# Optimization experiments

Hardware: AMD Instinct MI355X
Metric: run time of the kernel (lower is better)

Reference implementation:

```python
import jax, jax.numpy as jnp
import numpy as np

N, E, IN_DIM, HID, HEADS, LAYERS, NTYPES, NGRAPH = 50000, 600000, 64, 128, 8, 3, 10, 500
C = HID // HEADS
NEG_SLOPE = 0.2
EPS = 1e-5


def setup_inputs() -> dict:
    key = jax.random.key(0)
    ks = jax.random.split(key, 24)
    inp = {
        "x": jax.random.normal(ks[0], (N, IN_DIM), jnp.float32),
        "edge_index": jax.random.randint(ks[1], (2, E), 0, N),
        "node_types": jax.random.randint(ks[2], (N,), 0, NTYPES),
        "batch": jnp.sort(jax.random.randint(ks[3], (N,), 0, NGRAPH)),
        # node embedding linear
        "emb_W": jax.random.normal(ks[4], (IN_DIM, HID), jnp.float32) / np.sqrt(IN_DIM),
        "emb_b": jnp.zeros((HID,), jnp.float32),
        "ntype_emb": jax.random.normal(ks[5], (NTYPES, HID), jnp.float32) * 0.02,
        # stacked GAT layer params
        "gat_W": jax.random.normal(ks[6], (LAYERS, HID, HID), jnp.float32) / np.sqrt(HID),
        "att_src": jax.random.normal(ks[7], (LAYERS, HEADS, C), jnp.float32) * 0.1,
        "att_dst": jax.random.normal(ks[8], (LAYERS, HEADS, C), jnp.float32) * 0.1,
        "gat_b": jnp.zeros((LAYERS, HID), jnp.float32),
        "ln_g": jnp.ones((LAYERS, HID), jnp.float32),
        "ln_b": jnp.zeros((LAYERS, HID), jnp.float32),
        # global attention MLP
        "ga_W1": jax.random.normal(ks[9], (HID, HID), jnp.float32) / np.sqrt(HID),
        "ga_b1": jnp.zeros((HID,), jnp.float32),
        "ga_W2": jax.random.normal(ks[10], (HID, 1), jnp.float32) / np.sqrt(HID),
        "ga_b2": jnp.zeros((1,), jnp.float32),
        # graph classifier head
        "cls_W1": jax.random.normal(ks[11], (HID, HID), jnp.float32) / np.sqrt(HID),
        "cls_b1": jnp.zeros((HID,), jnp.float32),
        "cls_W2": jax.random.normal(ks[12], (HID, 1), jnp.float32) / np.sqrt(HID),
        "cls_b2": jnp.zeros((1,), jnp.float32),
    }
    return inp


def _layer_norm(h, g, b):
    mu = jnp.mean(h, axis=-1, keepdims=True)
    var = jnp.mean(jnp.square(h - mu), axis=-1, keepdims=True)
    return (h - mu) * jax.lax.rsqrt(var + EPS) * g + b


def _gat_layer(h, src, dst, W, a_src, a_dst, bias):
    # h: [N, HID] -> per-head projection [N, H, C]
    hp = (h @ W).reshape(N, HEADS, C)
    alpha_s = jnp.sum(hp * a_src, axis=-1)  # [N, H]
    alpha_d = jnp.sum(hp * a_dst, axis=-1)  # [N, H]
    e = jax.nn.leaky_relu(alpha_s[src] + alpha_d[dst], NEG_SLOPE)  # [E', H]
    # segment softmax over incoming edges of each destination node
    m = jax.ops.segment_max(e, dst, num_segments=N)
    ex = jnp.exp(e - m[dst])
    s = jax.ops.segment_sum(ex, dst, num_segments=N)
    alpha = ex / s[dst]  # every node has a self-loop, so s > 0
    msg = hp[src] * alpha[:, :, None]  # [E', H, C]
    out = jax.ops.segment_sum(msg, dst, num_segments=N)  # [N, H, C]
    return out.reshape(N, HID) + bias


def reference(x, edge_index, node_types, batch, emb_W, emb_b, ntype_emb,
              gat_W, att_src, att_dst, gat_b, ln_g, ln_b,
              ga_W1, ga_b1, ga_W2, ga_b2, cls_W1, cls_b1, cls_W2, cls_b2):
    # self-loops (PyG GATConv add_self_loops=True)
    loop = jnp.arange(N)
    src = jnp.concatenate([edge_index[0], loop])
    dst = jnp.concatenate([edge_index[1], loop])

    h = x @ emb_W + emb_b
    h = h + ntype_emb[node_types]

    for l in range(LAYERS):
        h_prev = h
        h = _gat_layer(h, src, dst, gat_W[l], att_src[l], att_dst[l], gat_b[l])
        h = _layer_norm(h, ln_g[l], ln_b[l])
        h = jax.nn.relu(h + h_prev)

    # global attention pooling: softmax over all nodes (dim 0, as in source)
    scores = jnp.tanh(h @ ga_W1 + ga_b1) @ ga_W2 + ga_b2  # [N, 1]
    attw = jax.nn.softmax(scores, axis=0)
    h_graph = jnp.sum(h * attw, axis=0)  # [HID]

    # global mean pool per graph
    sums = jax.ops.segment_sum(h, batch, num_segments=NGRAPH)  # [G, HID]
    cnts = jax.ops.segment_sum(jnp.ones((N, 1), h.dtype), batch, num_segments=NGRAPH)
    mean_pool = sums / jnp.maximum(cnts, 1.0)

    hg = h_graph + mean_pool  # broadcast [HID] + [G, HID]

    # graph classifier head (features_batch=None path), squeeze(-1)
    out = jax.nn.relu(hg @ cls_W1 + cls_b1) @ cls_W2 + cls_b2
    return out.squeeze(-1)  # [G]
```

## Files before the change

### kernel.cpp

```cpp
#include <hip/hip_runtime.h>
#include <hip/hip_bf16.h>
#include <math.h>

#define HID 128
#define HEADS 8
#define INDIM 64

typedef _Float16 f16x8 __attribute__((ext_vector_type(8)));
typedef _Float16 f16x4 __attribute__((ext_vector_type(4)));
typedef float f32x4 __attribute__((ext_vector_type(4)));

__device__ __forceinline__ float fast_tanh(float x) {
    return 1.f - 2.f / (__expf(2.f * x) + 1.f);
}


__global__ void count_kernel(const int* __restrict__ ei, int* __restrict__ deg, int E, int EE) {
    int e = blockIdx.x * blockDim.x + threadIdx.x;
    if (e >= EE) return;
    int dst = (e < E) ? ei[E + e] : (e - E);
    atomicAdd(&deg[dst], 1);
}

__global__ void block_sum_kernel(const int* __restrict__ deg, int* __restrict__ partials, int N) {
    __shared__ int sdata[4];
    int t = threadIdx.x;
    int i = blockIdx.x * 256 + t;
    int v = (i < N) ? deg[i] : 0;
#pragma unroll
    for (int m = 32; m >= 1; m >>= 1) v += __shfl_xor(v, m, 64);
    if ((t & 63) == 0) sdata[t >> 6] = v;
    __syncthreads();
    if (t == 0) partials[blockIdx.x] = sdata[0] + sdata[1] + sdata[2] + sdata[3];
}

__global__ void scan_partials_kernel(int* __restrict__ partials, int nb) {
    int lane = threadIdx.x;
    int carry = 0;
    for (int base = 0; base < nb; base += 64) {
        int i = base + lane;
        int v = (i < nb) ? partials[i] : 0;
        int orig = v;
#pragma unroll
        for (int off = 1; off < 64; off <<= 1) {
            int x = __shfl_up(v, off, 64);
            if (lane >= off) v += x;
        }
        if (i < nb) partials[i] = v - orig + carry;
        carry += __shfl(v, 63, 64);
    }
}

__global__ void rowptr_kernel(const int* __restrict__ deg, const int* __restrict__ partials,
                              int* __restrict__ rowptr, int* __restrict__ woff, int N, int EE) {
    __shared__ int tmp[256];
    int t = threadIdx.x;
    int i = blockIdx.x * 256 + t;
    int v = (i < N) ? deg[i] : 0;
    tmp[t] = v;
    __syncthreads();
#pragma unroll
    for (int off = 1; off < 256; off <<= 1) {
        int x = (t >= off) ? tmp[t - off] : 0;
        __syncthreads();
        tmp[t] += x;
        __syncthreads();
    }
    int excl = tmp[t] - v + partials[blockIdx.x];
    if (i < N) { rowptr[i] = excl; woff[i] = excl; }
    if (blockIdx.x == 0 && t == 0) rowptr[N] = EE;
}

__global__ void scatter_kernel(const int* __restrict__ ei, int* __restrict__ woff,
                               int* __restrict__ esrc, int E, int EE) {
    int e = blockIdx.x * blockDim.x + threadIdx.x;
    if (e >= EE) return;
    int src, dst;
    if (e < E) { src = ei[e]; dst = ei[E + e]; } else { src = dst = e - E; }
    int slot = atomicAdd(&woff[dst], 1);
    esrc[slot] = src;
}

__global__ void gstart_kernel(const int* __restrict__ batch, int* __restrict__ gstart,
                              int N, int G) {
    int g = blockIdx.x * blockDim.x + threadIdx.x;
    if (g > G) return;
    int lo = 0, hi = N;
    while (lo < hi) {
        int mid = (lo + hi) >> 1;
        if (batch[mid] < g) lo = mid + 1; else hi = mid;
    }
    gstart[g] = lo;
}

__global__ void convert_x_kernel(const float* __restrict__ x, _Float16* __restrict__ x16, int tot4) {
    int i = blockIdx.x * blockDim.x + threadIdx.x;
    if (i >= tot4) return;
    float4 v = ((const float4*)x)[i];
    f16x4 o; o[0] = (_Float16)v.x; o[1] = (_Float16)v.y; o[2] = (_Float16)v.z; o[3] = (_Float16)v.w;
    *(f16x4*)&x16[4 * i] = o;
}

__global__ void convert_w_kernel(const float* __restrict__ emb_W, const float* __restrict__ gat_W,
                                 const float* __restrict__ ga_W1, _Float16* __restrict__ wt_emb,
                                 _Float16* __restrict__ wt_gat, _Float16* __restrict__ wt_ga1) {
    int i = blockIdx.x * blockDim.x + threadIdx.x;
    if (i < 8192) {
        int k = i >> 7, n = i & 127;
        wt_emb[n * 64 + k] = (_Float16)emb_W[i];
    } else if (i < 8192 + 49152) {
        int j = i - 8192;
        int l = j >> 14, r = j & 16383;
        int k = r >> 7, n = r & 127;
        wt_gat[l * 16384 + n * 128 + k] = (_Float16)gat_W[j];
    } else if (i < 73728) {
        int j = i - 57344;
        int k = j >> 7, n = j & 127;
        wt_ga1[n * 128 + k] = (_Float16)ga_W1[j];
    }
}

__global__ __launch_bounds__(256) void mfma_proj_kernel(
    int mode, int K, int N,
    const _Float16* __restrict__ A16, const _Float16* __restrict__ Wt,
    const float* __restrict__ bias, const float* __restrict__ nemb,
    const int* __restrict__ ntypes, _Float16* __restrict__ h16out,
    const float* __restrict__ asrc, const float* __restrict__ adst,
    _Float16* __restrict__ hp_out, float* __restrict__ als, float* __restrict__ ald,
    const float* __restrict__ w2, const float* __restrict__ b2,
    float* __restrict__ escore)
{
    __shared__ _Float16 w_lds[128 * 136];
    int t = threadIdx.x;
    int n0 = blockIdx.x * 64;

    int K8 = K >> 3;
    for (int i = t; i < 128 * K8; i += 256) {
        int row = i / K8, c8 = i - row * K8;
        *(f16x8*)&w_lds[row * 136 + 8 * c8] = *(const f16x8*)&Wt[(size_t)row * K + 8 * c8];
    }
    __syncthreads();

    int lane = t & 63, wv = t >> 6;
    int l15 = lane & 15, quad = lane >> 4;
    int arow = n0 + wv * 16 + l15;
    if (arow > N - 1) arow = N - 1;

    f32x4 acc[8];
#pragma unroll
    for (int c = 0; c < 8; ++c) acc[c] = (f32x4){0.f, 0.f, 0.f, 0.f};

    int ksteps = K >> 5;
    for (int kk = 0; kk < ksteps; ++kk) {
        f16x8 af = *(const f16x8*)&A16[(size_t)arow * K + kk * 32 + quad * 8];
#pragma unroll
        for (int c = 0; c < 8; ++c) {
            f16x8 bf = *(const f16x8*)&w_lds[(c * 16 + l15) * 136 + kk * 32 + quad * 8];
            acc[c] = __builtin_amdgcn_mfma_f32_16x16x32_f16(af, bf, acc[c], 0, 0, 0);
        }
    }

    if (mode == 0) {
        float bv[8];
#pragma unroll
        for (int c = 0; c < 8; ++c) bv[c] = bias[c * 16 + l15];
        __syncthreads();
#pragma unroll
        for (int r = 0; r < 4; ++r) {
            int n = n0 + wv * 16 + quad * 4 + r;
            int nt = (n < N) ? ntypes[n] : 0;
#pragma unroll
            for (int c = 0; c < 8; ++c)
                w_lds[(wv * 16 + quad * 4 + r) * 136 + c * 16 + l15] =
                    (_Float16)(acc[c][r] + bv[c] + nemb[nt * HID + c * 16 + l15]);
        }
        __syncthreads();
        for (int i = t; i < 64 * 16; i += 256) {
            int row = i >> 4, c8 = i & 15;
            int n = n0 + row;
            if (n < N) *(f16x8*)&h16out[(size_t)n * HID + 8 * c8] = *(const f16x8*)&w_lds[row * 136 + 8 * c8];
        }
    } else if (mode == 1) {
#pragma unroll
        for (int c = 0; c < 8; ++c) {
            float asv = asrc[c * 16 + l15];
            float adv = adst[c * 16 + l15];
#pragma unroll
            for (int r = 0; r < 4; ++r) {
                float va = acc[c][r] * asv;
                float vd = acc[c][r] * adv;
#pragma unroll
                for (int m = 8; m >= 1; m >>= 1) {
                    va += __shfl_xor(va, m, 64);
                    vd += __shfl_xor(vd, m, 64);
                }
                if (l15 == 0) {
                    int n = n0 + wv * 16 + quad * 4 + r;
                    if (n < N) {
                        als[n * HEADS + c] = va;
                        ald[n * HEADS + c] = vd;
                    }
                }
            }
        }
        __syncthreads();
#pragma unroll
        for (int c = 0; c < 8; ++c)
#pragma unroll
            for (int r = 0; r < 4; ++r)
                w_lds[(wv * 16 + quad * 4 + r) * 136 + c * 16 + l15] = (_Float16)acc[c][r];
        __syncthreads();
        for (int i = t; i < 64 * 16; i += 256) {
            int row = i >> 4, c8 = i & 15;
            int n = n0 + row;
            if (n < N) *(f16x8*)&hp_out[(size_t)n * HID + 8 * c8] = *(const f16x8*)&w_lds[row * 136 + 8 * c8];
        }
    } else {
        float b2v = b2[0];
        float treg[4] = {0.f, 0.f, 0.f, 0.f};
#pragma unroll
        for (int c = 0; c < 8; ++c) {
            float b1v = bias[c * 16 + l15];
            float w2v = w2[c * 16 + l15];
#pragma unroll
            for (int r = 0; r < 4; ++r)
                treg[r] += fast_tanh(acc[c][r] + b1v) * w2v;
        }
#pragma unroll
        for (int r = 0; r < 4; ++r) {
            float v = treg[r];
#pragma unroll
            for (int m = 8; m >= 1; m >>= 1) v += __shfl_xor(v, m, 64);
            if (l15 == 0) {
                int n = n0 + wv * 16 + quad * 4 + r;
                if (n < N) escore[n] = __expf(v + b2v);
            }
        }
    }
}

__global__ void gat_aggregate_kernel(const int* __restrict__ rowptr, const int* __restrict__ esrc,
                                     const float* __restrict__ als, const float* __restrict__ ald,
                                     const _Float16* __restrict__ hp16, const float* __restrict__ gb,
                                     const float* __restrict__ lg, const float* __restrict__ lb,
                                     _Float16* __restrict__ h16, int N) {
    int wave = threadIdx.x >> 6;
    int lane = threadIdx.x & 63;
    int n = blockIdx.x * 4 + wave;
    if (n >= N) return;
    int esub = lane >> 4;
    int cg = lane & 15;
    int hd = cg >> 1;
    float adv = ald[n * HEADS + hd];
    int row = rowptr[n], end = rowptr[n + 1];
    int last = end - 1;
    float acc[8] = {0.f, 0.f, 0.f, 0.f, 0.f, 0.f, 0.f, 0.f};
    float sw = 0.f;
    for (int base = row; base < end; base += 8) {
        int iA = base + esub, iB = base + 4 + esub;
        int cA = iA <= last ? iA : last;
        int cB = iB <= last ? iB : last;
        int sA = esrc[cA], sB = esrc[cB];
        f16x8 pA = *(const f16x8*)&hp16[(size_t)sA * HID + cg * 8];
        f16x8 pB = *(const f16x8*)&hp16[(size_t)sB * HID + cg * 8];
        float aA = als[sA * HEADS + hd];
        float aB = als[sB * HEADS + hd];
        float mA = (iA < end) ? 1.f : 0.f;
        float mB = (iB < end) ? 1.f : 0.f;
        float lA = aA + adv; lA = lA > 0.f ? lA : 0.2f * lA;
        float lB = aB + adv; lB = lB > 0.f ? lB : 0.2f * lB;
        float wA = __expf(lA) * mA;
        float wB = __expf(lB) * mB;
        sw += wA + wB;
#pragma unroll
        for (int j = 0; j < 8; ++j)
            acc[j] += wA * (float)pA[j] + wB * (float)pB[j];
    }
#pragma unroll
    for (int m = 16; m <= 32; m <<= 1) {
        sw += __shfl_xor(sw, m, 64);
#pragma unroll
        for (int j = 0; j < 8; ++j) acc[j] += __shfl_xor(acc[j], m, 64);
    }
    float inv_sw = 1.f / sw;
    float4 g0 = ((const float4*)(gb + cg * 8))[0];
    float4 g1 = ((const float4*)(gb + cg * 8))[1];
    float v[8];
    v[0] = acc[0] * inv_sw + g0.x; v[1] = acc[1] * inv_sw + g0.y;
    v[2] = acc[2] * inv_sw + g0.z; v[3] = acc[3] * inv_sw + g0.w;
    v[4] = acc[4] * inv_sw + g1.x; v[5] = acc[5] * inv_sw + g1.y;
    v[6] = acc[6] * inv_sw + g1.z; v[7] = acc[7] * inv_sw + g1.w;
    float s = 0.f;
#pragma unroll
    for (int j = 0; j < 8; ++j) s += v[j];
#pragma unroll
    for (int m = 32; m >= 1; m >>= 1) s += __shfl_xor(s, m, 64);
    float mu = s * (1.f / 512.f);
    float d[8], sq = 0.f;
#pragma unroll
    for (int j = 0; j < 8; ++j) { d[j] = v[j] - mu; sq += d[j] * d[j]; }
#pragma unroll
    for (int m = 32; m >= 1; m >>= 1) sq += __shfl_xor(sq, m, 64);
    float inv = rsqrtf(sq * (1.f / 512.f) + 1e-5f);
    float4 lg0 = ((const float4*)(lg + cg * 8))[0];
    float4 lg1 = ((const float4*)(lg + cg * 8))[1];
    float4 lb0 = ((const float4*)(lb + cg * 8))[0];
    float4 lb1 = ((const float4*)(lb + cg * 8))[1];
    float lgv[8] = {lg0.x, lg0.y, lg0.z, lg0.w, lg1.x, lg1.y, lg1.z, lg1.w};
    float lbv[8] = {lb0.x, lb0.y, lb0.z, lb0.w, lb1.x, lb1.y, lb1.z, lb1.w};
    f16x8 hold = *(const f16x8*)&h16[(size_t)n * HID + cg * 8];
    f16x8 hnew;
#pragma unroll
    for (int j = 0; j < 8; ++j) {
        float r = d[j] * inv * lgv[j] + lbv[j] + (float)hold[j];
        hnew[j] = (_Float16)(r > 0.f ? r : 0.f);
    }
    if (esub == 0) *(f16x8*)&h16[(size_t)n * HID + cg * 8] = hnew;
}

__global__ void pool_graph_kernel(const _Float16* __restrict__ h16, const float* __restrict__ escore,
                                  const int* __restrict__ gstart, float* __restrict__ sums,
                                  float* __restrict__ cnts, float* __restrict__ hgZ, int G) {
    int g = blockIdx.x;
    int t = threadIdx.x;
    int c = t & 127, grp = t >> 7;
    int s = gstart[g], e = gstart[g + 1];
    float msum = 0.f, asum = 0.f, z = 0.f;
    for (int n = s + grp; n < e; n += 4) {
        float hv = (float)h16[(size_t)n * HID + c];
        float es = escore[n];
        msum += hv;
        asum += es * hv;
        if (c == 0) z += es;
    }
    __shared__ float sm[4][HID];
    __shared__ float sa[4][HID];
    __shared__ float sz[4];
    sm[grp][c] = msum;
    sa[grp][c] = asum;
    if (c == 0) sz[grp] = z;
    __syncthreads();
    if (t < HID) {
        float m = sm[0][t] + sm[1][t] + sm[2][t] + sm[3][t];
        float a = sa[0][t] + sa[1][t] + sa[2][t] + sa[3][t];
        sums[(size_t)g * HID + t] = m;
        atomicAdd(&hgZ[t], a);
    } else if (t == HID) {
        cnts[g] = (float)(e - s);
        atomicAdd(&hgZ[HID], sz[0] + sz[1] + sz[2] + sz[3]);
    }
}

__global__ void head_kernel(const float* __restrict__ hgZ, const float* __restrict__ sums,
                            const float* __restrict__ cnts, const float* __restrict__ W1,
                            const float* __restrict__ b1, const float* __restrict__ W2,
                            const float* __restrict__ b2, float* __restrict__ out, int G) {
    int g = blockIdx.x;
    int t = threadIdx.x;
    __shared__ float hr[HID];
    __shared__ float part[2];
    float Z = hgZ[HID];
    float cnt = cnts[g];
    cnt = cnt > 1.f ? cnt : 1.f;
    hr[t] = hgZ[t] / Z + sums[(size_t)g * HID + t] / cnt;
    __syncthreads();
    float acc = b1[t];
#pragma unroll 8
    for (int k = 0; k < HID; ++k) acc += hr[k] * W1[k * HID + t];
    acc = acc > 0.f ? acc : 0.f;
    float v = acc * W2[t];
#pragma unroll
    for (int m = 32; m >= 1; m >>= 1) v += __shfl_xor(v, m, 64);
    if ((t & 63) == 0) part[t >> 6] = v;
    __syncthreads();
    if (t == 0) out[g] = part[0] + part[1] + b2[0];
}

extern "C" void kernel_launch(void* const* d_in, const int* in_sizes, int n_in,
                              void* d_out, int out_size, void* d_ws, size_t ws_size,
                              hipStream_t stream) {
    const float* x        = (const float*)d_in[0];
    const int*   ei       = (const int*)d_in[1];
    const int*   ntypes   = (const int*)d_in[2];
    const int*   batch    = (const int*)d_in[3];
    const float* emb_W    = (const float*)d_in[4];
    const float* emb_b    = (const float*)d_in[5];
    const float* nemb     = (const float*)d_in[6];
    const float* gat_W    = (const float*)d_in[7];
    const float* att_src  = (const float*)d_in[8];
    const float* att_dst  = (const float*)d_in[9];
    const float* gat_b    = (const float*)d_in[10];
    const float* ln_g     = (const float*)d_in[11];
    const float* ln_b     = (const float*)d_in[12];
    const float* ga_W1    = (const float*)d_in[13];
    const float* ga_b1    = (const float*)d_in[14];
    const float* ga_W2    = (const float*)d_in[15];
    const float* ga_b2    = (const float*)d_in[16];
    const float* cls_W1   = (const float*)d_in[17];
    const float* cls_b1   = (const float*)d_in[18];
    const float* cls_W2   = (const float*)d_in[19];
    const float* cls_b2   = (const float*)d_in[20];
    float* out = (float*)d_out;

    const int N  = in_sizes[2];
    const int E  = in_sizes[1] / 2;
    const int EE = E + N;
    const int G  = out_size;
    const int NB = (N + 255) / 256;

    float* ws      = (float*)d_ws;
    float* als     = ws;
    float* ald     = als + (size_t)N * HEADS;
    float* escore  = ald + (size_t)N * HEADS;
    float* sums    = escore + N;
    float* cnts    = sums + (size_t)G * HID;
    float* hgZ     = cnts + G;
    _Float16* h16  = (_Float16*)(hgZ + HID + 1);
    _Float16* hp16 = h16 + (size_t)N * HID;
    _Float16* x16  = hp16 + (size_t)N * HID;
    _Float16* wt_emb = x16 + (size_t)N * INDIM;
    _Float16* wt_gat = wt_emb + 128 * 64;
    _Float16* wt_ga1 = wt_gat + 3 * 128 * 128;
    int*   rowptr  = (int*)(wt_ga1 + 128 * 128);
    int*   woff    = rowptr + (N + 1);
    int*   deg     = woff + N;
    int*   esrc    = deg + N;
    int*   partials= esrc + EE;
    int*   gstart  = partials + NB;

    hipMemsetAsync(deg, 0, (size_t)N * sizeof(int), stream);
    hipMemsetAsync(hgZ, 0, (HID + 1) * sizeof(float), stream);
    count_kernel<<<(EE + 255) / 256, 256, 0, stream>>>(ei, deg, E, EE);
    block_sum_kernel<<<NB, 256, 0, stream>>>(deg, partials, N);
    scan_partials_kernel<<<1, 64, 0, stream>>>(partials, NB);
    rowptr_kernel<<<NB, 256, 0, stream>>>(deg, partials, rowptr, woff, N, EE);
    scatter_kernel<<<(EE + 255) / 256, 256, 0, stream>>>(ei, woff, esrc, E, EE);
    gstart_kernel<<<(G + 64) / 64, 64, 0, stream>>>(batch, gstart, N, G);
    convert_x_kernel<<<(N * INDIM / 4 + 255) / 256, 256, 0, stream>>>(x, x16, N * INDIM / 4);
    convert_w_kernel<<<(73728 + 255) / 256, 256, 0, stream>>>(
        emb_W, gat_W, ga_W1, wt_emb, wt_gat, wt_ga1);

    const int PB = (N + 63) / 64;

    mfma_proj_kernel<<<PB, 256, 0, stream>>>(
        0, INDIM, N, x16, wt_emb, emb_b, nemb, ntypes, h16,
        nullptr, nullptr, nullptr, nullptr, nullptr, nullptr, nullptr, nullptr);

    for (int l = 0; l < 3; ++l) {
        mfma_proj_kernel<<<PB, 256, 0, stream>>>(
            1, HID, N, h16, wt_gat + (size_t)l * HID * HID,
            nullptr, nullptr, nullptr, nullptr,
            att_src + l * HID, att_dst + l * HID,
            hp16, als, ald, nullptr, nullptr, nullptr);
        gat_aggregate_kernel<<<(N + 3) / 4, 256, 0, stream>>>(
            rowptr, esrc, als, ald, hp16,
            gat_b + l * HID, ln_g + l * HID, ln_b + l * HID, h16, N);
    }

    mfma_proj_kernel<<<PB, 256, 0, stream>>>(
        2, HID, N, h16, wt_ga1, ga_b1, nullptr, nullptr, nullptr,
        nullptr, nullptr, nullptr, nullptr, nullptr, ga_W2, ga_b2, escore);

    pool_graph_kernel<<<G, 512, 0, stream>>>(h16, escore, gstart, sums, cnts, hgZ, G);
    head_kernel<<<G, 128, 0, stream>>>(hgZ, sums, cnts, cls_W1, cls_b1, cls_W2, cls_b2, out, G);
}
```

Baseline: 437.5 us.

## Stage A tile in LDS, compute attention logits from LDS, unroll edge aggregation 4x

The projection kernel now loads the 64-row A tile into shared memory with zero-fill instead of reading it from global memory inside the MFMA loop. The mode-1 attention logits are computed from the fp16 tile in LDS with per-thread dot products, replacing the shuffle reductions. The GAT aggregation loop processes four edges per lane per iteration and uses fdot2 on packed fp16 weights when available, which raises memory-level parallelism. The fdot2 path rounds attention weights to fp16, which can hurt accuracy or overflow for large exponentials, and the extra LDS may lower occupancy.

New measurement: 427.6 us. 1.02x faster.

```diff
diff --git a/kernel.cpp b/kernel.cpp
--- a/kernel.cpp
+++ b/kernel.cpp
@@ -8,11 +8,18 @@
 
 typedef _Float16 f16x8 __attribute__((ext_vector_type(8)));
 typedef _Float16 f16x4 __attribute__((ext_vector_type(4)));
+typedef _Float16 f16x2 __attribute__((ext_vector_type(2)));
 typedef float f32x4 __attribute__((ext_vector_type(4)));
 
 __device__ __forceinline__ float fast_tanh(float x) {
     return 1.f - 2.f / (__expf(2.f * x) + 1.f);
 }
+
+#if defined(__has_builtin)
+#if __has_builtin(__builtin_amdgcn_fdot2)
+#define HAVE_FDOT2 1
+#endif
+#endif
 
 
 __global__ void count_kernel(const int* __restrict__ ei, int* __restrict__ deg, int E, int EE) {
@@ -131,20 +138,26 @@
     float* __restrict__ escore)
 {
     __shared__ _Float16 w_lds[128 * 136];
+    __shared__ _Float16 a_lds[64 * 136];
     int t = threadIdx.x;
     int n0 = blockIdx.x * 64;
+    int KP = K + 8;
 
     int K8 = K >> 3;
     for (int i = t; i < 128 * K8; i += 256) {
         int row = i / K8, c8 = i - row * K8;
-        *(f16x8*)&w_lds[row * 136 + 8 * c8] = *(const f16x8*)&Wt[(size_t)row * K + 8 * c8];
+        *(f16x8*)&w_lds[row * KP + 8 * c8] = *(const f16x8*)&Wt[(size_t)row * K + 8 * c8];
+    }
+    for (int i = t; i < 64 * K8; i += 256) {
+        int row = i / K8, c8 = i - row * K8;
+        f16x8 v = {};
+        if (n0 + row < N) v = *(const f16x8*)&A16[(size_t)(n0 + row) * K + 8 * c8];
+        *(f16x8*)&a_lds[row * KP + 8 * c8] = v;
     }
     __syncthreads();
 
     int lane = t & 63, wv = t >> 6;
     int l15 = lane & 15, quad = lane >> 4;
-    int arow = n0 + wv * 16 + l15;
-    if (arow > N - 1) arow = N - 1;
 
     f32x4 acc[8];
 #pragma unroll
@@ -152,10 +165,10 @@
 
     int ksteps = K >> 5;
     for (int kk = 0; kk < ksteps; ++kk) {
-        f16x8 af = *(const f16x8*)&A16[(size_t)arow * K + kk * 32 + quad * 8];
+        f16x8 af = *(const f16x8*)&a_lds[(wv * 16 + l15) * KP + kk * 32 + quad * 8];
 #pragma unroll
         for (int c = 0; c < 8; ++c) {
-            f16x8 bf = *(const f16x8*)&w_lds[(c * 16 + l15) * 136 + kk * 32 + quad * 8];
+            f16x8 bf = *(const f16x8*)&w_lds[(c * 16 + l15) * KP + kk * 32 + quad * 8];
             acc[c] = __builtin_amdgcn_mfma_f32_16x16x32_f16(af, bf, acc[c], 0, 0, 0);
         }
     }
@@ -171,49 +184,42 @@
             int nt = (n < N) ? ntypes[n] : 0;
 #pragma unroll
             for (int c = 0; c < 8; ++c)
-                w_lds[(wv * 16 + quad * 4 + r) * 136 + c * 16 + l15] =
+                a_lds[(wv * 16 + quad * 4 + r) * 136 + c * 16 + l15] =
                     (_Float16)(acc[c][r] + bv[c] + nemb[nt * HID + c * 16 + l15]);
         }
         __syncthreads();
         for (int i = t; i < 64 * 16; i += 256) {
             int row = i >> 4, c8 = i & 15;
             int n = n0 + row;
-            if (n < N) *(f16x8*)&h16out[(size_t)n * HID + 8 * c8] = *(const f16x8*)&w_lds[row * 136 + 8 * c8];
+            if (n < N) *(f16x8*)&h16out[(size_t)n * HID + 8 * c8] = *(const f16x8*)&a_lds[row * 136 + 8 * c8];
         }
     } else if (mode == 1) {
-#pragma unroll
-        for (int c = 0; c < 8; ++c) {
-            float asv = asrc[c * 16 + l15];
-            float adv = adst[c * 16 + l15];
-#pragma unroll
-            for (int r = 0; r < 4; ++r) {
-                float va = acc[c][r] * asv;
-                float vd = acc[c][r] * adv;
-#pragma unroll
-                for (int m = 8; m >= 1; m >>= 1) {
-                    va += __shfl_xor(va, m, 64);
-                    vd += __shfl_xor(vd, m, 64);
-                }
-                if (l15 == 0) {
-                    int n = n0 + wv * 16 + quad * 4 + r;
-                    if (n < N) {
-                        als[n * HEADS + c] = va;
-                        ald[n * HEADS + c] = vd;
-                    }
-                }
-            }
-        }
         __syncthreads();
 #pragma unroll
         for (int c = 0; c < 8; ++c)
 #pragma unroll
             for (int r = 0; r < 4; ++r)
-                w_lds[(wv * 16 + quad * 4 + r) * 136 + c * 16 + l15] = (_Float16)acc[c][r];
+                a_lds[(wv * 16 + quad * 4 + r) * 136 + c * 16 + l15] = (_Float16)acc[c][r];
         __syncthreads();
         for (int i = t; i < 64 * 16; i += 256) {
             int row = i >> 4, c8 = i & 15;
             int n = n0 + row;
-            if (n < N) *(f16x8*)&hp_out[(size_t)n * HID + 8 * c8] = *(const f16x8*)&w_lds[row * 136 + 8 * c8];
+            if (n < N) *(f16x8*)&hp_out[(size_t)n * HID + 8 * c8] = *(const f16x8*)&a_lds[row * 136 + 8 * c8];
+        }
+        for (int task = t; task < 512; task += 256) {
+            int row = task >> 3, hd = task & 7;
+            int n = n0 + row;
+            if (n >= N) continue;
+            f16x8 v0 = *(const f16x8*)&a_lds[row * 136 + hd * 16];
+            f16x8 v1 = *(const f16x8*)&a_lds[row * 136 + hd * 16 + 8];
+            float va = 0.f, vd = 0.f;
+#pragma unroll
+            for (int j = 0; j < 8; ++j) {
+                va += (float)v0[j] * asrc[hd * 16 + j] + (float)v1[j] * asrc[hd * 16 + 8 + j];
+                vd += (float)v0[j] * adst[hd * 16 + j] + (float)v1[j] * adst[hd * 16 + 8 + j];
+            }
+            als[n * HEADS + hd] = va;
+            ald[n * HEADS + hd] = vd;
         }
     } else {
         float b2v = b2[0];
@@ -256,25 +262,47 @@
     int last = end - 1;
     float acc[8] = {0.f, 0.f, 0.f, 0.f, 0.f, 0.f, 0.f, 0.f};
     float sw = 0.f;
-    for (int base = row; base < end; base += 8) {
-        int iA = base + esub, iB = base + 4 + esub;
+    for (int base = row; base < end; base += 16) {
+        int iA = base + esub;
+        int iB = iA + 4, iC = iA + 8, iD = iA + 12;
         int cA = iA <= last ? iA : last;
         int cB = iB <= last ? iB : last;
-        int sA = esrc[cA], sB = esrc[cB];
+        int cC = iC <= last ? iC : last;
+        int cD = iD <= last ? iD : last;
+        int sA = esrc[cA], sB = esrc[cB], sC = esrc[cC], sD = esrc[cD];
         f16x8 pA = *(const f16x8*)&hp16[(size_t)sA * HID + cg * 8];
         f16x8 pB = *(const f16x8*)&hp16[(size_t)sB * HID + cg * 8];
+        f16x8 pC = *(const f16x8*)&hp16[(size_t)sC * HID + cg * 8];
+        f16x8 pD = *(const f16x8*)&hp16[(size_t)sD * HID + cg * 8];
         float aA = als[sA * HEADS + hd];
         float aB = als[sB * HEADS + hd];
-        float mA = (iA < end) ? 1.f : 0.f;
-        float mB = (iB < end) ? 1.f : 0.f;
+        float aC = als[sC * HEADS + hd];
+        float aD = als[sD * HEADS + hd];
         float lA = aA + adv; lA = lA > 0.f ? lA : 0.2f * lA;
         float lB = aB + adv; lB = lB > 0.f ? lB : 0.2f * lB;
-        float wA = __expf(lA) * mA;
-        float wB = __expf(lB) * mB;
-        sw += wA + wB;
+        float lC = aC + adv; lC = lC > 0.f ? lC : 0.2f * lC;
+        float lD = aD + adv; lD = lD > 0.f ? lD : 0.2f * lD;
+        float wA = __expf(lA) * ((iA < end) ? 1.f : 0.f);
+        float wB = __expf(lB) * ((iB < end) ? 1.f : 0.f);
+        float wC = __expf(lC) * ((iC < end) ? 1.f : 0.f);
+        float wD = __expf(lD) * ((iD < end) ? 1.f : 0.f);
+        sw += (wA + wB) + (wC + wD);
+#ifdef HAVE_FDOT2
+        f16x2 wAB; wAB[0] = (_Float16)wA; wAB[1] = (_Float16)wB;
+        f16x2 wCD; wCD[0] = (_Float16)wC; wCD[1] = (_Float16)wD;
+#pragma unroll
+        for (int j = 0; j < 8; ++j) {
+            f16x2 prAB; prAB[0] = pA[j]; prAB[1] = pB[j];
+            f16x2 prCD; prCD[0] = pC[j]; prCD[1] = pD[j];
+            acc[j] = __builtin_amdgcn_fdot2(prAB, wAB, acc[j], false);
+            acc[j] = __builtin_amdgcn_fdot2(prCD, wCD, acc[j], false);
+        }
+#else
 #pragma unroll
         for (int j = 0; j < 8; ++j)
-            acc[j] += wA * (float)pA[j] + wB * (float)pB[j];
+            acc[j] += wA * (float)pA[j] + wB * (float)pB[j]
+                    + wC * (float)pC[j] + wD * (float)pD[j];
+#endif
     }
 #pragma unroll
     for (int m = 16; m <= 32; m <<= 1) {
```
